# Optimization experiments

Hardware: AMD Instinct MI355X
Metric: run time of the kernel (lower is better)

## Reference

```python
import jax, jax.numpy as jnp
import numpy as np

NUM_FRIENDS = 100000  # padding index == NUM_FRIENDS


def setup_inputs() -> dict:
    key = jax.random.key(0)
    ks = jax.random.split(key, 6)
    B, CLIP, D = 16384, 50, 64
    NU, NI = 100000, 100000
    user_indices = jax.random.randint(ks[0], (B,), 0, NU)
    item_indices = jax.random.randint(ks[1], (B,), 0, NI)
    # friend table; value NUM_FRIENDS acts as padding slot
    user_friend_indices = jax.random.randint(ks[2], (NU, CLIP), 0, NUM_FRIENDS + 1)
    emb_user = jax.random.normal(ks[3], (NUM_FRIENDS + 1, D), jnp.float32) * 0.1
    emb_user = emb_user.at[NUM_FRIENDS].set(0.0)  # padding_idx row is zero
    emb_item = jax.random.normal(ks[4], (NI, D), jnp.float32) * 0.1
    affine_w = jax.random.normal(ks[5], (D,), jnp.float32) * 0.1
    affine_b = jnp.zeros((), jnp.float32)
    return {
        "user_indices": user_indices,
        "item_indices": item_indices,
        "user_friend_indices": user_friend_indices,
        "emb_user": emb_user,
        "emb_item": emb_item,
        "affine_w": affine_w,
        "affine_b": affine_b,
    }


def reference(user_indices, item_indices, user_friend_indices, emb_user, emb_item, affine_w, affine_b):
    # gather friend ids: [B, CLIP]
    fi = user_friend_indices[user_indices]
    mask = (fi != NUM_FRIENDS)  # True = real friend
    clip = fi.shape[1]
    # friend embeddings, padding rows forced to zero (padding_idx semantics): [B, CLIP, D]
    fe = emb_user[fi] * mask[..., None].astype(emb_user.dtype)
    # number of real friends per user: [B, 1]
    friend_num = (clip - (~mask).sum(axis=1, keepdims=True)).astype(fe.dtype)
    ie = emb_item[item_indices]  # [B, D]
    # per-friend attention gate: sigmoid(linear(item_emb * friend_emb)) -> [B, CLIP, 1]
    group_idx = jax.nn.sigmoid(
        jnp.einsum('bcd,bd,d->bc', fe, ie, affine_w) + affine_b
    )[..., None]
    fe = fe * group_idx  # group=True path
    user_emb = fe.sum(axis=1) / friend_num  # [B, D]
    logits = jnp.einsum('bd,d->b', user_emb * ie, affine_w) + affine_b
    rating = jax.nn.sigmoid(logits)  # [B]
    return rating, group_idx
```

## Files before the change

### kernel.cpp

```cpp
#include <hip/hip_runtime.h>
#include <math.h>

#define BATCH      16384
#define CLIP       50
#define DIM        64
#define PAD_IDX    100000
#define NITER      13

__global__ __launch_bounds__(256) void gmf_kernel(
    const int*   __restrict__ user_indices,
    const int*   __restrict__ item_indices,
    const int*   __restrict__ user_friend_indices,
    const float* __restrict__ emb_user,
    const float* __restrict__ emb_item,
    const float* __restrict__ affine_w,
    const float* __restrict__ affine_b,
    float*       __restrict__ out)
{
    const int wave = (blockIdx.x * blockDim.x + threadIdx.x) >> 6;
    const int lane = threadIdx.x & 63;
    if (wave >= BATCH) return;

    const int b   = wave;
    const int sub = lane >> 4;
    const int li  = lane & 15;

    const int u  = user_indices[b];
    const int it = item_indices[b];
    const float bias = affine_b[0];

    const float4 ie = *(const float4*)(emb_item + (size_t)it * DIM + li * 4);
    const float4 w4 = *(const float4*)(affine_w + li * 4);
    float4 v;
    v.x = ie.x * w4.x; v.y = ie.y * w4.y; v.z = ie.z * w4.z; v.w = ie.w * w4.w;

    const int* fi_row = user_friend_indices + (size_t)u * CLIP;

    int fidx[NITER];
    #pragma unroll
    for (int i = 0; i < NITER; ++i) {
        const int c = 4 * i + sub;
        fidx[i] = (c < CLIP) ? fi_row[c] : PAD_IDX;
    }

    float4 fe[NITER];
    #pragma unroll
    for (int i = 0; i < NITER; ++i)
        fe[i] = *(const float4*)(emb_user + (size_t)fidx[i] * DIM + li * 4);

    float4 acc = make_float4(0.f, 0.f, 0.f, 0.f);
    float gkeep = 0.f;
    float cl    = 0.f;

    #pragma unroll
    for (int i = 0; i < NITER; ++i) {
        float p = fe[i].x * v.x + fe[i].y * v.y + fe[i].z * v.z + fe[i].w * v.w;
        p += __shfl_xor(p, 1, 64);
        p += __shfl_xor(p, 2, 64);
        p += __shfl_xor(p, 4, 64);
        p += __shfl_xor(p, 8, 64);

        const float g = 1.0f / (1.0f + __expf(-(p + bias)));

        acc.x += fe[i].x * g; acc.y += fe[i].y * g;
        acc.z += fe[i].z * g; acc.w += fe[i].w * g;

        if (li == i) gkeep = g;
        cl += (fidx[i] != PAD_IDX) ? 1.0f : 0.0f;
    }

    float cntf = cl;
    cntf += __shfl_xor(cntf, 16, 64);
    cntf += __shfl_xor(cntf, 32, 64);

    float q = acc.x * v.x + acc.y * v.y + acc.z * v.z + acc.w * v.w;
    q += __shfl_xor(q, 1, 64);
    q += __shfl_xor(q, 2, 64);
    q += __shfl_xor(q, 4, 64);
    q += __shfl_xor(q, 8, 64);
    q += __shfl_xor(q, 16, 64);
    q += __shfl_xor(q, 32, 64);

    const float rating = 1.0f / (1.0f + __expf(-(q / cntf + bias)));

    if (lane == 0)
        out[b] = rating;

    const int c = 4 * li + sub;
    if (c < CLIP)
        out[BATCH + (size_t)b * CLIP + c] = gkeep;
}

extern "C" void kernel_launch(void* const* d_in, const int* in_sizes, int n_in,
                              void* d_out, int out_size, void* d_ws, size_t ws_size,
                              hipStream_t stream) {
    const int*   user_indices        = (const int*)  d_in[0];
    const int*   item_indices        = (const int*)  d_in[1];
    const int*   user_friend_indices = (const int*)  d_in[2];
    const float* emb_user            = (const float*)d_in[3];
    const float* emb_item            = (const float*)d_in[4];
    const float* affine_w            = (const float*)d_in[5];
    const float* affine_b            = (const float*)d_in[6];
    float*       out                 = (float*)d_out;

    const int threads = 256;
    const int blocks  = (BATCH * 64) / threads;
    gmf_kernel<<<blocks, threads, 0, stream>>>(
        user_indices, item_indices, user_friend_indices,
        emb_user, emb_item, affine_w, affine_b, out);
}
```

Measured before the change: 127.5 us.

## Use rolling prefetch buffer and vectorized index loads to raise occupancy

Replaces the 13-deep register array of friend embeddings with a 6-slot rolling prefetch buffer, so fewer registers are live and the launch bound can request 8 waves per EU. Friend index loads become int4/int2 vector loads with per-sub-wave lane selection. It also adds a minimum-occupancy hint to launch bounds. The goal is more waves in flight to hide gather latency, at the cost of fewer outstanding loads per wave.

```diff
diff --git a/kernel.cpp b/kernel.cpp
--- a/kernel.cpp
+++ b/kernel.cpp
@@ -6,8 +6,9 @@
 #define DIM        64
 #define PAD_IDX    100000
 #define NITER      13
+#define PF         6
 
-__global__ __launch_bounds__(256) void gmf_kernel(
+__global__ __launch_bounds__(256, 8) void gmf_kernel(
     const int*   __restrict__ user_indices,
     const int*   __restrict__ item_indices,
     const int*   __restrict__ user_friend_indices,
@@ -36,17 +37,21 @@
 
     const int* fi_row = user_friend_indices + (size_t)u * CLIP;
 
-    int fidx[NITER];
+    int ids[NITER];
     #pragma unroll
-    for (int i = 0; i < NITER; ++i) {
-        const int c = 4 * i + sub;
-        fidx[i] = (c < CLIP) ? fi_row[c] : PAD_IDX;
+    for (int i = 0; i < 12; ++i) {
+        const int4 q = *(const int4*)(fi_row + 4 * i);
+        ids[i] = (sub == 0) ? q.x : (sub == 1) ? q.y : (sub == 2) ? q.z : q.w;
+    }
+    {
+        const int2 q = *(const int2*)(fi_row + 48);
+        ids[12] = (sub == 0) ? q.x : (sub == 1) ? q.y : PAD_IDX;
     }
 
-    float4 fe[NITER];
+    float4 fe[PF];
     #pragma unroll
-    for (int i = 0; i < NITER; ++i)
-        fe[i] = *(const float4*)(emb_user + (size_t)fidx[i] * DIM + li * 4);
+    for (int i = 0; i < PF; ++i)
+        fe[i] = *(const float4*)(emb_user + (size_t)ids[i] * DIM + li * 4);
 
     float4 acc = make_float4(0.f, 0.f, 0.f, 0.f);
     float gkeep = 0.f;
@@ -54,7 +59,11 @@
 
     #pragma unroll
     for (int i = 0; i < NITER; ++i) {
-        float p = fe[i].x * v.x + fe[i].y * v.y + fe[i].z * v.z + fe[i].w * v.w;
+        const float4 cur = fe[i % PF];
+        if (i + PF < NITER)
+            fe[i % PF] = *(const float4*)(emb_user + (size_t)ids[i + PF] * DIM + li * 4);
+
+        float p = cur.x * v.x + cur.y * v.y + cur.z * v.z + cur.w * v.w;
         p += __shfl_xor(p, 1, 64);
         p += __shfl_xor(p, 2, 64);
         p += __shfl_xor(p, 4, 64);
@@ -62,11 +71,11 @@
 
         const float g = 1.0f / (1.0f + __expf(-(p + bias)));
 
-        acc.x += fe[i].x * g; acc.y += fe[i].y * g;
-        acc.z += fe[i].z * g; acc.w += fe[i].w * g;
+        acc.x += cur.x * g; acc.y += cur.y * g;
+        acc.z += cur.z * g; acc.w += cur.w * g;
 
         if (li == i) gkeep = g;
-        cl += (fidx[i] != PAD_IDX) ? 1.0f : 0.0f;
+        cl += (ids[i] != PAD_IDX) ? 1.0f : 0.0f;
     }
 
     float cntf = cl;
```

New measurement: 179.1 us. 40.4% more time.

## Split each batch row's friends across two waves with shared-memory reduction

Applied to the files above, without the earlier changes.

Each batch element is now handled by two waves, each gathering and gating half of the 50 friends (25 each, 7 iterations instead of 13). Partial dot products and friend counts are combined through shared memory after a block barrier. The friend-index load and the embedding gather are also merged into one loop. This doubles the number of waves so more gathers are in flight and fewer registers are needed per wave, at the cost of a __syncthreads, duplicated item-embedding loads, and some wasted padding slots.

```diff
diff --git a/kernel.cpp b/kernel.cpp
--- a/kernel.cpp
+++ b/kernel.cpp
@@ -1,11 +1,12 @@
 #include <hip/hip_runtime.h>
 #include <math.h>
 
-#define BATCH      16384
-#define CLIP       50
-#define DIM        64
-#define PAD_IDX    100000
-#define NITER      13
+#define BATCH    16384
+#define CLIP     50
+#define DIM      64
+#define PAD_IDX  100000
+#define HALF     25
+#define NIT      7
 
 __global__ __launch_bounds__(256) void gmf_kernel(
     const int*   __restrict__ user_indices,
@@ -17,43 +18,41 @@
     const float* __restrict__ affine_b,
     float*       __restrict__ out)
 {
-    const int wave = (blockIdx.x * blockDim.x + threadIdx.x) >> 6;
-    const int lane = threadIdx.x & 63;
-    if (wave >= BATCH) return;
+    const int tid  = threadIdx.x;
+    const int lane = tid & 63;
+    const int wv   = (tid >> 6) & 1;
+    const int eb   = tid >> 7;
+    const int b    = blockIdx.x * 2 + eb;
 
-    const int b   = wave;
     const int sub = lane >> 4;
     const int li  = lane & 15;
 
     const int u  = user_indices[b];
     const int it = item_indices[b];
+
+    const int* fi_row = user_friend_indices + (size_t)u * CLIP + wv * HALF;
+
+    float  cl = 0.f;
+    float4 fe[NIT];
+    #pragma unroll
+    for (int i = 0; i < NIT; ++i) {
+        const int c = 4 * i + sub;
+        const int f = (c < HALF) ? fi_row[c] : PAD_IDX;
+        cl += (f != PAD_IDX) ? 1.f : 0.f;
+        fe[i] = *(const float4*)(emb_user + (size_t)f * DIM + li * 4);
+    }
+
     const float bias = affine_b[0];
-
     const float4 ie = *(const float4*)(emb_item + (size_t)it * DIM + li * 4);
     const float4 w4 = *(const float4*)(affine_w + li * 4);
     float4 v;
     v.x = ie.x * w4.x; v.y = ie.y * w4.y; v.z = ie.z * w4.z; v.w = ie.w * w4.w;
 
-    const int* fi_row = user_friend_indices + (size_t)u * CLIP;
-
-    int fidx[NITER];
-    #pragma unroll
-    for (int i = 0; i < NITER; ++i) {
-        const int c = 4 * i + sub;
-        fidx[i] = (c < CLIP) ? fi_row[c] : PAD_IDX;
-    }
-
-    float4 fe[NITER];
-    #pragma unroll
-    for (int i = 0; i < NITER; ++i)
-        fe[i] = *(const float4*)(emb_user + (size_t)fidx[i] * DIM + li * 4);
-
     float4 acc = make_float4(0.f, 0.f, 0.f, 0.f);
     float gkeep = 0.f;
-    float cl    = 0.f;
 
     #pragma unroll
-    for (int i = 0; i < NITER; ++i) {
+    for (int i = 0; i < NIT; ++i) {
         float p = fe[i].x * v.x + fe[i].y * v.y + fe[i].z * v.z + fe[i].w * v.w;
         p += __shfl_xor(p, 1, 64);
         p += __shfl_xor(p, 2, 64);
@@ -66,12 +65,11 @@
         acc.z += fe[i].z * g; acc.w += fe[i].w * g;
 
         if (li == i) gkeep = g;
-        cl += (fidx[i] != PAD_IDX) ? 1.0f : 0.0f;
     }
 
-    float cntf = cl;
-    cntf += __shfl_xor(cntf, 16, 64);
-    cntf += __shfl_xor(cntf, 32, 64);
+    float cntw = cl;
+    cntw += __shfl_xor(cntw, 16, 64);
+    cntw += __shfl_xor(cntw, 32, 64);
 
     float q = acc.x * v.x + acc.y * v.y + acc.z * v.z + acc.w * v.w;
     q += __shfl_xor(q, 1, 64);
@@ -81,14 +79,22 @@
     q += __shfl_xor(q, 16, 64);
     q += __shfl_xor(q, 32, 64);
 
-    const float rating = 1.0f / (1.0f + __expf(-(q / cntf + bias)));
+    __shared__ float red[2][2][2];
+    if (lane == 0) {
+        red[eb][wv][0] = q;
+        red[eb][wv][1] = cntw;
+    }
+    __syncthreads();
 
-    if (lane == 0)
-        out[b] = rating;
+    if (wv == 0 && lane == 0) {
+        const float qt = red[eb][0][0] + red[eb][1][0];
+        const float ct = red[eb][0][1] + red[eb][1][1];
+        out[b] = 1.0f / (1.0f + __expf(-(qt / ct + bias)));
+    }
 
     const int c = 4 * li + sub;
-    if (c < CLIP)
-        out[BATCH + (size_t)b * CLIP + c] = gkeep;
+    if (c < HALF)
+        out[BATCH + (size_t)b * CLIP + wv * HALF + c] = gkeep;
 }
 
 extern "C" void kernel_launch(void* const* d_in, const int* in_sizes, int n_in,
@@ -104,7 +110,7 @@
     float*       out                 = (float*)d_out;
 
     const int threads = 256;
-    const int blocks  = (BATCH * 64) / threads;
+    const int blocks  = BATCH / 2;
     gmf_kernel<<<blocks, threads, 0, stream>>>(
         user_indices, item_indices, user_friend_indices,
         emb_user, emb_item, affine_w, affine_b, out);
```

After: 127.4 us. Within noise of the previous version (-0.1%).
